# Optimization experiments

Measured on AMD Instinct MI355X. Metric: run time of the kernel, lower is better.

The kernel has to match this reference:

```python
import jax, jax.numpy as jnp
import numpy as np

NH = 8      # num_head
WIN = 7     # window
EPS = 1e-6


def _ln(x, w, b):
    m = x.mean(-1, keepdims=True)
    v = ((x - m) ** 2).mean(-1, keepdims=True)
    return (x - m) / jnp.sqrt(v + EPS) * w + b


def _dwconv(x, w, b):
    # x: [B,H,W,Cc], w: [7,7,1,Cc] (HWIO), depthwise (groups=Cc)
    y = jax.lax.conv_general_dilated(
        x, w, window_strides=(1, 1), padding='SAME',
        dimension_numbers=('NHWC', 'HWIO', 'NHWC'),
        feature_group_count=x.shape[-1])
    return y + b


def setup_inputs() -> dict:
    B, H, W, C = 16, 56, 56, 256
    RATIO = 8
    key = jax.random.key(0)
    ki = iter(jax.random.split(key, 48))
    def lin(i, o):
        return jax.random.normal(next(ki), (i, o), jnp.float32) * (1.0 / i) ** 0.5
    def bias(o):
        return jnp.zeros((o,), jnp.float32)
    def dw(c):
        return jax.random.normal(next(ki), (7, 7, 1, c), jnp.float32) * 0.05
    inp = {
        'x':   jax.random.normal(next(ki), (B, H, W, C), jnp.float32),
        'x_e': jax.random.normal(next(ki), (B, H, W, C // 2), jnp.float32),
        # LayerNorms
        'norm_w': jnp.ones((C,), jnp.float32),  'norm_b': bias(C),
        'norme_w': jnp.ones((C // 2,), jnp.float32), 'norme_b': bias(C // 2),
        # local_rr path
        'rr1_w': lin(C, C), 'rr1_b': bias(C),
        'rr2_w': lin(C, C), 'rr2_b': bias(C),
        'rr3_w': lin(C, C), 'rr3_b': bias(C),
        'conv_w': dw(C), 'conv_b': bias(C),
        # LocalAttentionRGBT
        'lx_l1_w': lin(C, C // 2), 'lx_l1_b': bias(C // 2),
        'lx_l2_w': lin(C // 2, C // 2), 'lx_l2_b': bias(C // 2),
        'lx_c1_w': dw(C // 2), 'lx_c1_b': bias(C // 2),
        'lx_c2_w': dw(C // 2), 'lx_c2_b': bias(C // 2),
        'lx_fc1_w': lin(C, C // RATIO),  # no bias
        'lx_fc2_w': lin(C // RATIO, C),  # no bias
        'lx_l3_w': lin(C, C // 2), 'lx_l3_b': bias(C // 2),
        # global pooled attention
        'kv_w': lin(C, C), 'kv_b': bias(C),
        'q_w': lin(C // 2 * 3, C // 2), 'q_b': bias(C // 2),
        # output projections (window != 0 => in = 2C)
        'proj_w': lin(2 * C, C), 'proj_b': bias(C),
        'proje_w': lin(2 * C, C // 2), 'proje_b': bias(C // 2),
    }
    return inp


def reference(x, x_e, norm_w, norm_b, norme_w, norme_b,
              rr1_w, rr1_b, rr2_w, rr2_b, rr3_w, rr3_b, conv_w, conv_b,
              lx_l1_w, lx_l1_b, lx_l2_w, lx_l2_b, lx_c1_w, lx_c1_b,
              lx_c2_w, lx_c2_b, lx_fc1_w, lx_fc2_w, lx_l3_w, lx_l3_b,
              kv_w, kv_b, q_w, q_b, proj_w, proj_b, proje_w, proje_b):
    B, H, W, C = x.shape
    hd = C // NH // 2  # head dim
    x = _ln(x, norm_w, norm_b)
    x_e = _ln(x_e, norme_w, norme_b)

    # --- local_rr: gated depthwise-conv branch ---
    rr1 = x @ rr1_w + rr1_b
    rr2 = _dwconv(x @ rr2_w + rr2_b, conv_w, conv_b)
    rr2 = rr2 @ rr3_w + rr3_b
    local_rr = rr1 * rr2  # [B,H,W,C]

    # --- LocalAttentionRGBT: cross-modal cosine-sim channel gate ---
    rgb = x @ lx_l1_w + lx_l1_b      # [B,H,W,C/2]
    t = x_e @ lx_l2_w + lx_l2_b      # [B,H,W,C/2]
    co = _dwconv(rgb * t, lx_c1_w, lx_c1_b)
    di = _dwconv(jnp.abs(rgb - t), lx_c2_w, lx_c2_b)
    co_di = jnp.concatenate([co, di], axis=-1)           # [B,H,W,C]
    amap = co_di.mean(-1, keepdims=True)                 # [B,H,W,1]
    dot = (amap * co_di).sum((1, 2), keepdims=True)      # [B,1,1,C]
    n1 = jnp.sqrt((amap ** 2).sum((1, 2), keepdims=True))
    n2 = jnp.sqrt((co_di ** 2).sum((1, 2), keepdims=True))
    cos_sim = dot / (n1 * n2 + 1e-6)                     # [B,1,1,C]
    attn_c = jax.nn.sigmoid(
        jax.nn.gelu(cos_sim @ lx_fc1_w, approximate=False) @ lx_fc2_w)
    local_rx = (co_di * attn_c) @ lx_l3_w + lx_l3_b      # [B,H,W,C/2]

    # --- global: pooled-q full-kv attention ---
    kv = (x @ kv_w + kv_b).reshape(B, H * W, 2, NH, hd).transpose(2, 0, 3, 1, 4)
    k, v = kv[0], kv[1]                                  # [B,NH,HW,hd]
    rx = jnp.concatenate([x, x_e], axis=-1)              # [B,H,W,3C/2]
    rx_pool = rx.reshape(B, WIN, H // WIN, WIN, W // WIN, -1).mean((2, 4))  # [B,7,7,3C/2]
    q = (rx_pool @ q_w + q_b).reshape(B, WIN * WIN, NH, hd).transpose(0, 2, 1, 3)
    scores = jnp.einsum('bnqd,bnkd->bnqk', q * hd ** -0.5, k)  # [B,NH,49,HW]
    attn = jax.nn.softmax(scores, axis=-1)
    g = jnp.einsum('bnqk,bnkd->bnqd', attn, v)           # [B,NH,49,hd]
    g = g.reshape(B, NH, WIN, WIN, hd).transpose(0, 1, 4, 2, 3).reshape(B, C // 2, WIN, WIN)
    g = jax.image.resize(g, (B, C // 2, H, W), method='bilinear')  # align_corners=False
    g = g.transpose(0, 2, 3, 1)                          # [B,H,W,C/2]

    cat = jnp.concatenate([local_rr, local_rx, g], axis=-1)  # [B,H,W,2C]
    x_e_out = cat @ proje_w + proje_b
    x_out = cat @ proj_w + proj_b
    return (x_out, x_e_out)
```

## Files before the change

### kernel.cpp

```cpp
#include <hip/hip_runtime.h>
#include <hip/hip_bf16.h>
#include <cstdint>
#include <cstddef>

#define N_TOK 50176
#define HWSZ  3136
#define BATCH 16

#define GF_MUL     1
#define GF_ASCALE  2
#define GF_KVSPLIT 4
#define GF_DUAL    8
#define GF_TRI     16
#define GF_RGBT    32

typedef __hip_bfloat16 bf16;
typedef __attribute__((ext_vector_type(8))) short bf16x8;
typedef __attribute__((ext_vector_type(4))) float f32x4;
typedef __attribute__((ext_vector_type(4))) unsigned short u16x4;

__device__ __forceinline__ void  stf(float* p, size_t i, float v) { p[i] = v; }
__device__ __forceinline__ void  stf(bf16* p, size_t i, float v) { p[i] = __float2bfloat16(v); }
__device__ __forceinline__ float bu2f(unsigned short u) {
    unsigned int x = ((unsigned int)u) << 16; float f; __builtin_memcpy(&f, &x, 4); return f;
}
__device__ __forceinline__ unsigned short f2bu(float f) {
    bf16 t = __float2bfloat16(f); unsigned short u; __builtin_memcpy(&u, &t, 2); return u;
}

struct WtrDesc { const float* src; bf16* dst; int K; int N; int off; };
struct WtrPack { WtrDesc d[9]; int total; };
__global__ __launch_bounds__(256) void wtr_all(WtrPack p)
{
    int idx = blockIdx.x * 256 + threadIdx.x;
    if (idx >= p.total) return;
    #pragma unroll
    for (int s = 0; s < 9; s++) {
        int lo = p.d[s].off, hi = lo + p.d[s].K * p.d[s].N;
        if (idx >= lo && idx < hi) {
            int j = idx - lo;
            int k = j / p.d[s].N, n = j % p.d[s].N;
            p.d[s].dst[(size_t)n * p.d[s].K + k] = __float2bfloat16(p.d[s].src[j]);
        }
    }
}

__global__ __launch_bounds__(256) void ln_kernel(const float* __restrict__ in,
    const float* __restrict__ w, const float* __restrict__ b,
    bf16* __restrict__ out, int rows, int Cdim)
{
    int wave = threadIdx.x >> 6, lane = threadIdx.x & 63;
    int row = blockIdx.x * 4 + wave;
    if (row >= rows) return;
    const float* p = in + (size_t)row * Cdim;
    int nj = Cdim >> 6;
    float v[4];
    float s = 0.f;
    for (int j = 0; j < nj; j++) { v[j] = p[lane + 64 * j]; s += v[j]; }
    for (int off = 32; off; off >>= 1) s += __shfl_xor(s, off, 64);
    float mean = s / (float)Cdim;
    float vs = 0.f;
    for (int j = 0; j < nj; j++) { float d = v[j] - mean; vs += d * d; }
    for (int off = 32; off; off >>= 1) vs += __shfl_xor(vs, off, 64);
    float rstd = 1.f / sqrtf(vs / (float)Cdim + 1e-6f);
    bf16* q = out + (size_t)row * Cdim;
    for (int j = 0; j < nj; j++) {
        int c = lane + 64 * j;
        q[c] = __float2bfloat16((v[j] - mean) * rstd * w[c] + b[c]);
    }
}

#define LDT 40
template<int FLAGS, typename OT>
__global__ __launch_bounds__(256) void gemm_mfma(
    const bf16* __restrict__ A, int lda,
    const bf16* __restrict__ WT,
    const float* __restrict__ bias,
    OT* __restrict__ C, int ldc,
    int M, int K, int N,
    const bf16* __restrict__ mul, int mulld,
    const float* __restrict__ ascale,
    bf16* __restrict__ kout, bf16* __restrict__ vout,
    OT* __restrict__ C2, int ldc2, const float* __restrict__ bias2, int N1)
{
    __shared__ bf16 As[2][64][LDT];
    __shared__ bf16 Bs[2][128][LDT];
    int ntile = N >> 7;
    int bid = blockIdx.x;
    bid = (bid & 7) * (gridDim.x >> 3) + (bid >> 3);
    int m0 = (bid / ntile) * 64;
    int n0 = (bid % ntile) * 128;
    int tid = threadIdx.x;
    int lane = tid & 63, wid = tid >> 6;
    int wc = wid * 32;
    int lrow = lane & 15, lko = (lane >> 4) * 8;
    int sr = tid >> 2, sko = (tid & 3) * 8;

    f32x4 acc[4][2];
    #pragma unroll
    for (int i = 0; i < 4; i++)
        #pragma unroll
        for (int j = 0; j < 2; j++)
            acc[i][j] = (f32x4){0.f, 0.f, 0.f, 0.f};

#define GLOAD(RA, RB0, RB1, KOFF) do {                                                        \
    bf16x8 v_ = *reinterpret_cast<const bf16x8*>(A + (size_t)(m0 + sr) * lda + (KOFF) + sko); \
    if (FLAGS & GF_ASCALE) {                                                                  \
        int bidx_ = (m0 + sr) / HWSZ;                                                         \
        const float* as_ = ascale + (size_t)bidx_ * K + (KOFF) + sko;                         \
        for (int e_ = 0; e_ < 8; e_++)                                                        \
            v_[e_] = (short)f2bu(bu2f((unsigned short)v_[e_]) * as_[e_]);                     \
    }                                                                                         \
    RA = v_;                                                                                  \
    RB0 = *reinterpret_cast<const bf16x8*>(WT + (size_t)(n0 + sr) * K + (KOFF) + sko);        \
    RB1 = *reinterpret_cast<const bf16x8*>(WT + (size_t)(n0 + sr + 64) * K + (KOFF) + sko);   \
} while (0)

#define GWRITE(P, RA, RB0, RB1) do {                                   \
    *reinterpret_cast<bf16x8*>(&As[P][sr][sko]) = RA;                  \
    *reinterpret_cast<bf16x8*>(&Bs[P][sr][sko]) = RB0;                 \
    *reinterpret_cast<bf16x8*>(&Bs[P][sr + 64][sko]) = RB1;            \
} while (0)

#define GCOMP(P) do {                                                                         \
    bf16x8 af_[4], br_[2];                                                                    \
    for (int i_ = 0; i_ < 4; i_++)                                                            \
        af_[i_] = *reinterpret_cast<const bf16x8*>(&As[P][i_ * 16 + lrow][lko]);              \
    for (int j_ = 0; j_ < 2; j_++)                                                            \
        br_[j_] = *reinterpret_cast<const bf16x8*>(&Bs[P][wc + j_ * 16 + lrow][lko]);         \
    for (int i_ = 0; i_ < 4; i_++)                                                            \
        for (int j_ = 0; j_ < 2; j_++)                                                        \
            acc[i_][j_] = __builtin_amdgcn_mfma_f32_16x16x32_bf16(af_[i_], br_[j_], acc[i_][j_], 0, 0, 0); \
} while (0)

    bf16x8 ra0, rb00, rb01, ra1, rb10, rb11;
    GLOAD(ra0, rb00, rb01, 0);
    GLOAD(ra1, rb10, rb11, 32);
    int nst = K >> 5;
    for (int s = 0; s < nst; s += 2) {
        GWRITE(0, ra0, rb00, rb01);
        if (s + 2 < nst) GLOAD(ra0, rb00, rb01, (s + 2) * 32);
        __syncthreads();
        GCOMP(0);
        GWRITE(1, ra1, rb10, rb11);
        if (s + 3 < nst) GLOAD(ra1, rb10, rb11, (s + 3) * 32);
        __syncthreads();
        GCOMP(1);
    }
#undef GLOAD
#undef GWRITE
#undef GCOMP

    int orow = (lane >> 4) * 4;
    int ocol = lane & 15;
    #pragma unroll
    for (int i = 0; i < 4; i++) {
        #pragma unroll
        for (int j = 0; j < 2; j++) {
            #pragma unroll
            for (int p = 0; p < 4; p++) {
                int gm = m0 + i * 16 + orow + p;
                int gn = n0 + wc + j * 16 + ocol;
                if (FLAGS & GF_TRI) {
                    if (gn < 256) {
                        stf(C, (size_t)gm * ldc + gn, acc[i][j][p] + bias[gn]);
                    } else if (gn < 512) {
                        stf(C2, (size_t)gm * ldc2 + (gn - 256), acc[i][j][p] + bias2[gn - 256]);
                    } else {
                        int g3 = gn - 512;
                        float v = acc[i][j][p] + ascale[g3];
                        int bb = gm / HWSZ, n = gm % HWSZ;
                        if (g3 < 128)
                            kout[(((size_t)bb * 8 + (g3 >> 4)) * HWSZ + n) * 16 + (g3 & 15)] = __float2bfloat16(v);
                        else {
                            int hh = (g3 - 128) >> 4, dd = (g3 - 128) & 15;
                            vout[(((size_t)bb * 8 + hh) * 16 + dd) * HWSZ + n] = __float2bfloat16(v);
                        }
                    }
                } else if (FLAGS & GF_RGBT) {
                    float t = acc[i][j][p] + bias[gn];
                    float rgb = __bfloat162float(mul[(size_t)gm * mulld + gn]);
                    stf(C, (size_t)gm * ldc + gn, rgb * t);
                    stf(C, (size_t)gm * ldc + 128 + gn, fabsf(rgb - t));
                } else if (FLAGS & GF_KVSPLIT) {
                    float v = acc[i][j][p] + bias[gn];
                    int bb = gm / HWSZ, n = gm % HWSZ;
                    if (gn < 128)
                        kout[(((size_t)bb * 8 + (gn >> 4)) * HWSZ + n) * 16 + (gn & 15)] = __float2bfloat16(v);
                    else {
                        int hh = (gn - 128) >> 4, dd = (gn - 128) & 15;
                        vout[(((size_t)bb * 8 + hh) * 16 + dd) * HWSZ + n] = __float2bfloat16(v);
                    }
                } else if (FLAGS & GF_DUAL) {
                    if (gn < N1) {
                        float v = acc[i][j][p] + bias[gn];
                        stf(C, (size_t)gm * ldc + gn, v);
                    } else {
                        float v = acc[i][j][p] + bias2[gn - N1];
                        stf(C2, (size_t)gm * ldc2 + (gn - N1), v);
                    }
                } else {
                    float v = acc[i][j][p] + bias[gn];
                    if (FLAGS & GF_MUL) v *= __bfloat162float(mul[(size_t)gm * mulld + gn]);
                    stf(C, (size_t)gm * ldc + gn, v);
                }
            }
        }
    }
}

__global__ __launch_bounds__(256) void gemm_k(
    const float* __restrict__ A, int lda,
    const float* __restrict__ Wt, const float* __restrict__ bias,
    float* __restrict__ Cc, int ldc, int M, int K, int Nc)
{
    __shared__ float As[16][68];
    __shared__ float Ws[16][64];
    int ntile = Nc >> 6;
    int tile_n = blockIdx.x % ntile;
    int tile_m = blockIdx.x / ntile;
    int m0 = tile_m * 64, n0 = tile_n * 64;
    int tid = threadIdx.x;
    int tx = tid & 15, ty = tid >> 4;
    float acc[4][4] = {};
    for (int k0 = 0; k0 < K; k0 += 16) {
        int ks = tid & 15, ms = tid >> 4;
        #pragma unroll
        for (int i = 0; i < 4; i++) {
            int gm = m0 + ms + i * 16;
            As[ks][ms + i * 16] = (gm < M) ? A[(size_t)gm * lda + k0 + ks] : 0.f;
        }
        #pragma unroll
        for (int j = 0; j < 4; j++) {
            int k = (tid >> 6) * 4 + j;
            Ws[k][tid & 63] = Wt[(size_t)(k0 + k) * Nc + n0 + (tid & 63)];
        }
        __syncthreads();
        #pragma unroll
        for (int k = 0; k < 16; k++) {
            float a[4], w[4];
            #pragma unroll
            for (int i = 0; i < 4; i++) a[i] = As[k][ty * 4 + i];
            #pragma unroll
            for (int j = 0; j < 4; j++) w[j] = Ws[k][tx * 4 + j];
            #pragma unroll
            for (int i = 0; i < 4; i++)
                #pragma unroll
                for (int j = 0; j < 4; j++)
                    acc[i][j] += a[i] * w[j];
        }
        __syncthreads();
    }
    #pragma unroll
    for (int i = 0; i < 4; i++) {
        int gm = m0 + ty * 4 + i;
        if (gm >= M) continue;
        #pragma unroll
        for (int j = 0; j < 4; j++) {
            int gn = n0 + tx * 4 + j;
            Cc[(size_t)gm * ldc + gn] = acc[i][j] + bias[gn];
        }
    }
}

__global__ __launch_bounds__(256) void dwconv_reg(const bf16* __restrict__ in,
    bf16* __restrict__ out,
    const float* __restrict__ w0, const float* __restrict__ b0,
    const float* __restrict__ w1, const float* __restrict__ b1, int split)
{
    int tid = threadIdx.x;
    int chg = tid & 31;
    int bsw = (blockIdx.x & 7) * 196 + (blockIdx.x >> 3);
    int pg  = bsw * 8 + (tid >> 5);
    int xg = pg % 14;
    int y  = (pg / 14) % 56;
    int b  = pg / (14 * 56);
    int c0 = chg * 8;
    int x0 = xg * 4;

    const float* wp; const float* bp; int ws, cw;
    if (c0 < split) { wp = w0; bp = b0; ws = split;       cw = c0; }
    else            { wp = w1; bp = b1; ws = 256 - split; cw = c0 - split; }

    float acc[4][8];
    #pragma unroll
    for (int o = 0; o < 4; o++)
        #pragma unroll
        for (int e = 0; e < 8; e++) acc[o][e] = 0.f;

    const bf16* base = in + (size_t)b * HWSZ * 256 + c0;
    const float* wbase = wp + cw;
    #pragma unroll
    for (int ky = 0; ky < 7; ky++) {
        int gy = y + ky - 3;
        if (gy < 0 || gy >= 56) continue;
        const bf16* rowp = base + (size_t)gy * 56 * 256;
        float cf[10][8];
        #pragma unroll
        for (int j = 0; j < 10; j++) {
            int gx = x0 + j - 3;
            bf16x8 v = {0, 0, 0, 0, 0, 0, 0, 0};
            if ((unsigned)gx < 56u)
                v = *reinterpret_cast<const bf16x8*>(rowp + (size_t)gx * 256);
            #pragma unroll
            for (int e = 0; e < 8; e++) cf[j][e] = bu2f((unsigned short)v[e]);
        }
        const float* wrow = wbase + ky * 7 * ws;
        #pragma unroll
        for (int kx = 0; kx < 7; kx++) {
            float4 wa = *reinterpret_cast<const float4*>(wrow + kx * ws);
            float4 wb = *reinterpret_cast<const float4*>(wrow + kx * ws + 4);
            #pragma unroll
            for (int o = 0; o < 4; o++) {
                acc[o][0] += cf[o + kx][0] * wa.x;
                acc[o][1] += cf[o + kx][1] * wa.y;
                acc[o][2] += cf[o + kx][2] * wa.z;
                acc[o][3] += cf[o + kx][3] * wa.w;
                acc[o][4] += cf[o + kx][4] * wb.x;
                acc[o][5] += cf[o + kx][5] * wb.y;
                acc[o][6] += cf[o + kx][6] * wb.z;
                acc[o][7] += cf[o + kx][7] * wb.w;
            }
        }
    }

    float4 ba = *reinterpret_cast<const float4*>(bp + cw);
    float4 bb = *reinterpret_cast<const float4*>(bp + cw + 4);
    bf16* obase = out + (((size_t)b * HWSZ + (size_t)y * 56 + x0) * 256) + c0;
    #pragma unroll
    for (int o = 0; o < 4; o++) {
        bf16x8 ov;
        ov[0] = (short)f2bu(acc[o][0] + ba.x);
        ov[1] = (short)f2bu(acc[o][1] + ba.y);
        ov[2] = (short)f2bu(acc[o][2] + ba.z);
        ov[3] = (short)f2bu(acc[o][3] + ba.w);
        ov[4] = (short)f2bu(acc[o][4] + bb.x);
        ov[5] = (short)f2bu(acc[o][5] + bb.y);
        ov[6] = (short)f2bu(acc[o][6] + bb.z);
        ov[7] = (short)f2bu(acc[o][7] + bb.w);
        *reinterpret_cast<bf16x8*>(obase + (size_t)o * 256) = ov;
    }
}

__global__ __launch_bounds__(256) void cosred_k(const bf16* __restrict__ codi,
    float* __restrict__ part)
{
    int b = blockIdx.x >> 4;
    int bi = blockIdx.x & 15;
    int wave = threadIdx.x >> 6, lane = threadIdx.x & 63;
    int slot = bi * 4 + wave;
    float dloc[4] = {0,0,0,0}, n2loc[4] = {0,0,0,0};
    float n1loc = 0.f;
    for (int i = 0; i < 49; i++) {
        int p = slot * 49 + i;
        const bf16* row = codi + ((size_t)b * HWSZ + p) * 256;
        float v[4]; float sum = 0.f;
        #pragma unroll
        for (int j = 0; j < 4; j++) { v[j] = __bfloat162float(row[lane + 64 * j]); sum += v[j]; }
        for (int off = 32; off; off >>= 1) sum += __shfl_xor(sum, off, 64);
        float amap = sum * (1.f / 256.f);
        #pragma unroll
        for (int j = 0; j < 4; j++) { dloc[j] += amap * v[j]; n2loc[j] += v[j] * v[j]; }
        n1loc += amap * amap;
    }
    float* dst = part + ((size_t)b * 64 + slot) * 513;
    #pragma unroll
    for (int j = 0; j < 4; j++) {
        dst[lane + 64 * j] = dloc[j];
        dst[256 + lane + 64 * j] = n2loc[j];
    }
    if (lane == 0) dst[512] = n1loc;
}

__global__ __launch_bounds__(256) void mlp_kernel(const float* __restrict__ part,
    const float* __restrict__ fc1w, const float* __restrict__ fc2w,
    float* __restrict__ attnc)
{
    int b = blockIdx.x;
    int tid = threadIdx.x;
    __shared__ float cosb[256];
    __shared__ float hbuf[32];
    const float* pb = part + (size_t)b * 64 * 513;
    float dot = 0.f, n2 = 0.f, n1 = 0.f;
    for (int s = 0; s < 64; s++) {
        dot += pb[s * 513 + tid];
        n2  += pb[s * 513 + 256 + tid];
        n1  += pb[s * 513 + 512];
    }
    float cs = dot / (sqrtf(n1) * sqrtf(n2) + 1e-6f);
    cosb[tid] = cs;
    __syncthreads();
    if (tid < 32) {
        float h = 0.f;
        for (int c = 0; c < 256; c++) h += cosb[c] * fc1w[c * 32 + tid];
        h = 0.5f * h * (1.f + erff(h * 0.70710678f));
        hbuf[tid] = h;
    }
    __syncthreads();
    float o = 0.f;
    for (int j = 0; j < 32; j++) o += hbuf[j] * fc2w[j * 256 + tid];
    attnc[b * 256 + tid] = 1.f / (1.f + expf(-o));
}

__global__ __launch_bounds__(384) void pool_kernel(const bf16* __restrict__ xn,
    const bf16* __restrict__ xen, float* __restrict__ rxpool)
{
    int bij = blockIdx.x;
    int b = bij / 49; int ij = bij % 49; int i = ij / 7, j = ij % 7;
    int c = threadIdx.x;
    float s = 0.f;
    for (int dy = 0; dy < 8; dy++)
        for (int dx = 0; dx < 8; dx++) {
            size_t n = ((size_t)b * 56 + (i * 8 + dy)) * 56 + (j * 8 + dx);
            s += (c < 256) ? __bfloat162float(xn[n * 256 + c])
                           : __bfloat162float(xen[n * 128 + (c - 256)]);
        }
    rxpool[(size_t)bij * 384 + c] = s * (1.f / 64.f);
}

#define NSPLIT 14
#define POSB   224
__global__ __launch_bounds__(256) void attn_mfma(const float* __restrict__ qbuf,
    const bf16* __restrict__ kbuf, const bf16* __restrict__ vtbuf,
    float* __restrict__ osplit, float* __restrict__ mlbuf)
{
    int bh = blockIdx.x & 127;
    int split = blockIdx.x >> 7;
    int b = bh >> 3, h = bh & 7;
    int tid = threadIdx.x;
    int qt = tid >> 6;
    int lane = tid & 63;
    int lo = lane & 15, hi = lane >> 4;

    bf16x8 qf = {0, 0, 0, 0, 0, 0, 0, 0};
    int q = qt * 16 + lo;
    if (hi < 2 && q < 49) {
        const float* qp = qbuf + ((size_t)b * 49 + q) * 128 + h * 16 + hi * 8;
        #pragma unroll
        for (int j = 0; j < 8; j++) qf[j] = (short)f2bu(qp[j] * 0.25f);
    }
    const bf16* kbase = kbuf + (size_t)bh * HWSZ * 16;
    const bf16* vbase = vtbuf + ((size_t)bh * 16 + lo) * HWSZ;

    float m_run = -1e30f, l_run = 0.f;
    f32x4 oacc = {0.f, 0.f, 0.f, 0.f};
    int pos1 = 8 * (lo >> 2) + (lo & 3);
    const f32x4 zz = {0.f, 0.f, 0.f, 0.f};

    for (int t = 0; t < POSB / 32; t++) {
        int base = split * POSB + t * 32;
        bf16x8 kf1 = {0, 0, 0, 0, 0, 0, 0, 0}, kf2 = kf1;
        if (hi < 2) {
            kf1 = *reinterpret_cast<const bf16x8*>(kbase + (size_t)(base + pos1) * 16 + hi * 8);
            kf2 = *reinterpret_cast<const bf16x8*>(kbase + (size_t)(base + pos1 + 4) * 16 + hi * 8);
        }
        bf16x8 vf = *reinterpret_cast<const bf16x8*>(vbase + base + hi * 8);
        f32x4 s1 = __builtin_amdgcn_mfma_f32_16x16x32_bf16(kf1, qf, zz, 0, 0, 0);
        f32x4 s2 = __builtin_amdgcn_mfma_f32_16x16x32_bf16(kf2, qf, zz, 0, 0, 0);
        float pmax = fmaxf(fmaxf(fmaxf(s1[0], s1[1]), fmaxf(s1[2], s1[3])),
                           fmaxf(fmaxf(s2[0], s2[1]), fmaxf(s2[2], s2[3])));
        pmax = fmaxf(pmax, __shfl_xor(pmax, 16, 64));
        pmax = fmaxf(pmax, __shfl_xor(pmax, 32, 64));
        float mnew = fmaxf(m_run, pmax);
        float esc = __expf(m_run - mnew);
        l_run *= esc;
        float e0 = __shfl(esc, 4 * hi + 0, 64);
        float e1 = __shfl(esc, 4 * hi + 1, 64);
        float e2 = __shfl(esc, 4 * hi + 2, 64);
        float e3 = __shfl(esc, 4 * hi + 3, 64);
        oacc[0] *= e0; oacc[1] *= e1; oacc[2] *= e2; oacc[3] *= e3;
        float p0 = __expf(s1[0] - mnew), p1 = __expf(s1[1] - mnew);
        float p2 = __expf(s1[2] - mnew), p3 = __expf(s1[3] - mnew);
        float p4 = __expf(s2[0] - mnew), p5 = __expf(s2[1] - mnew);
        float p6 = __expf(s2[2] - mnew), p7 = __expf(s2[3] - mnew);
        float rs = ((p0 + p1) + (p2 + p3)) + ((p4 + p5) + (p6 + p7));
        rs += __shfl_xor(rs, 16, 64);
        rs += __shfl_xor(rs, 32, 64);
        l_run += rs;
        m_run = mnew;
        bf16x8 pf;
        pf[0] = (short)f2bu(p0); pf[1] = (short)f2bu(p1);
        pf[2] = (short)f2bu(p2); pf[3] = (short)f2bu(p3);
        pf[4] = (short)f2bu(p4); pf[5] = (short)f2bu(p5);
        pf[6] = (short)f2bu(p6); pf[7] = (short)f2bu(p7);
        oacc = __builtin_amdgcn_mfma_f32_16x16x32_bf16(pf, vf, oacc, 0, 0, 0);
    }

    float* ob = osplit + ((size_t)bh * NSPLIT + split) * 64 * 16;
    #pragma unroll
    for (int r = 0; r < 4; r++) {
        int qq = qt * 16 + 4 * hi + r;
        ob[(size_t)qq * 16 + lo] = oacc[r];
    }
    if (hi == 0) {
        float* mlb = mlbuf + (((size_t)bh * NSPLIT + split) * 64 + qt * 16 + lo) * 2;
        mlb[0] = m_run; mlb[1] = l_run;
    }
}

__global__ __launch_bounds__(256) void attn_combine(const float* __restrict__ osplit,
    const float* __restrict__ mlbuf, float* __restrict__ gs)
{
    int idx = blockIdx.x * 256 + threadIdx.x;
    if (idx >= 128 * 49 * 16) return;
    int d = idx & 15;
    int pq = idx >> 4;
    int bh = pq / 49, q = pq % 49;
    float m[NSPLIT], l[NSPLIT];
    float M = -1e30f;
    #pragma unroll
    for (int s = 0; s < NSPLIT; s++) {
        const float* mlb = mlbuf + (((size_t)bh * NSPLIT + s) * 64 + q) * 2;
        m[s] = mlb[0]; l[s] = mlb[1];
        M = fmaxf(M, m[s]);
    }
    float L = 0.f, O = 0.f;
    #pragma unroll
    for (int s = 0; s < NSPLIT; s++) {
        float e = __expf(m[s] - M);
        L += l[s] * e;
        O += osplit[(((size_t)bh * NSPLIT + s) * 64 + q) * 16 + d] * e;
    }
    gs[(size_t)pq * 16 + d] = O / L;
}

__global__ void upsample_kernel(const float* __restrict__ gs, bf16* __restrict__ cat)
{
    int idx = blockIdx.x * blockDim.x + threadIdx.x;
    if (idx >= N_TOK * 128) return;
    int c = idx & 127;
    int pos = idx >> 7;
    int h = c >> 4, d = c & 15;
    int x = pos % 56;
    int y = (pos / 56) % 56;
    int b = pos / HWSZ;
    float sy = (y + 0.5f) * 0.125f - 0.5f;
    float sx = (x + 0.5f) * 0.125f - 0.5f;
    int y0f = (int)floorf(sy); float wy = sy - (float)y0f;
    int x0f = (int)floorf(sx); float wx = sx - (float)x0f;
    int y0 = max(0, min(6, y0f)), y1 = max(0, min(6, y0f + 1));
    int x0 = max(0, min(6, x0f)), x1 = max(0, min(6, x0f + 1));
    const float* g0 = gs + ((size_t)(b * 8 + h) * 49) * 16 + d;
    float v00 = g0[(y0 * 7 + x0) * 16], v01 = g0[(y0 * 7 + x1) * 16];
    float v10 = g0[(y1 * 7 + x0) * 16], v11 = g0[(y1 * 7 + x1) * 16];
    float v0 = v00 + (v01 - v00) * wx;
    float v1 = v10 + (v11 - v10) * wx;
    float v = v0 + (v1 - v0) * wy;
    cat[(size_t)pos * 512 + 384 + c] = __float2bfloat16(v);
}

extern "C" void kernel_launch(void* const* d_in, const int* in_sizes, int n_in,
                              void* d_out, int out_size, void* d_ws, size_t ws_size,
                              hipStream_t stream)
{
    const float* x      = (const float*)d_in[0];
    const float* x_e    = (const float*)d_in[1];
    const float* norm_w = (const float*)d_in[2];
    const float* norm_b = (const float*)d_in[3];
    const float* norme_w= (const float*)d_in[4];
    const float* norme_b= (const float*)d_in[5];
    const float* rr1_w  = (const float*)d_in[6];
    const float* rr1_b  = (const float*)d_in[7];
    const float* rr2_w  = (const float*)d_in[8];
    const float* rr2_b  = (const float*)d_in[9];
    const float* rr3_w  = (const float*)d_in[10];
    const float* rr3_b  = (const float*)d_in[11];
    const float* conv_w = (const float*)d_in[12];
    const float* conv_b = (const float*)d_in[13];
    const float* l1_w   = (const float*)d_in[14];
    const float* l1_b   = (const float*)d_in[15];
    const float* l2_w   = (const float*)d_in[16];
    const float* l2_b   = (const float*)d_in[17];
    const float* c1_w   = (const float*)d_in[18];
    const float* c1_b   = (const float*)d_in[19];
    const float* c2_w   = (const float*)d_in[20];
    const float* c2_b   = (const float*)d_in[21];
    const float* fc1_w  = (const float*)d_in[22];
    const float* fc2_w  = (const float*)d_in[23];
    const float* l3_w   = (const float*)d_in[24];
    const float* l3_b   = (const float*)d_in[25];
    const float* kv_w   = (const float*)d_in[26];
    const float* kv_b   = (const float*)d_in[27];
    const float* q_w    = (const float*)d_in[28];
    const float* q_b    = (const float*)d_in[29];
    const float* proj_w = (const float*)d_in[30];
    const float* proj_b = (const float*)d_in[31];
    const float* proje_w= (const float*)d_in[32];
    const float* proje_b= (const float*)d_in[33];

    float* part   = (float*)d_ws;
    float* attnc  = part   + (size_t)525312;
    float* gs     = attnc  + 4096;
    float* rxpool = gs     + 100352;
    float* qbuf   = rxpool + 301056;
    bf16* wt      = (bf16*)(qbuf + 100352);
    bf16* rr1_t  = wt;
    bf16* rr2_t  = rr1_t + 65536;
    bf16* kv_t   = rr2_t + 65536;
    bf16* rr3_t  = kv_t  + 65536;
    bf16* l1_t   = rr3_t + 65536;
    bf16* l2_t   = l1_t  + 32768;
    bf16* l3_t   = l2_t  + 16384;
    bf16* proj_t = l3_t  + 32768;
    bf16* proje_t= proj_t + 131072;
    bf16* xn     = proje_t + 65536;
    bf16* xen    = xn   + (size_t)N_TOK * 256;
    bf16* bufC   = xen  + (size_t)N_TOK * 128;
    bf16* bufD   = bufC + (size_t)N_TOK * 256;
    bf16* bufE   = bufD + (size_t)N_TOK * 256;
    bf16* cat    = bufE + (size_t)N_TOK * 256;
    bf16* kvbuf  = cat  + (size_t)N_TOK * 512;
    size_t need = (size_t)((char*)(kvbuf + (size_t)N_TOK * 256) - (char*)d_ws);
    if (ws_size < need) return;

    bf16* kbuf = kvbuf;
    bf16* vbuf = kvbuf + (size_t)N_TOK * 128;

    float* osplit = (float*)bufD;
    float* mlbuf  = osplit + (size_t)128 * NSPLIT * 64 * 16;

    float* xout  = (float*)d_out;
    float* xeout = xout + (size_t)N_TOK * 256;

    const int nthr = 256;
    auto mgrid = [](int M, int N) { return dim3((M / 64) * (N / 128)); };

    {
        WtrPack p;
        const float* srcs[9] = {rr1_w, rr2_w, kv_w, rr3_w, l1_w, l2_w, l3_w, proj_w, proje_w};
        bf16* dsts[9] = {rr1_t, rr2_t, kv_t, rr3_t, l1_t, l2_t, l3_t, proj_t, proje_t};
        int Ks[9] = {256, 256, 256, 256, 256, 128, 256, 512, 512};
        int Ns[9] = {256, 256, 256, 256, 128, 128, 128, 256, 128};
        int off = 0;
        for (int s = 0; s < 9; s++) {
            p.d[s] = {srcs[s], dsts[s], Ks[s], Ns[s], off};
            off += Ks[s] * Ns[s];
        }
        p.total = off;
        wtr_all<<<dim3((off + 255) / 256), dim3(256), 0, stream>>>(p);
    }

    ln_kernel<<<dim3(N_TOK / 4), dim3(nthr), 0, stream>>>(x, norm_w, norm_b, xn, N_TOK, 256);
    ln_kernel<<<dim3(N_TOK / 4), dim3(nthr), 0, stream>>>(x_e, norme_w, norme_b, xen, N_TOK, 128);

    gemm_mfma<GF_TRI, bf16><<<mgrid(N_TOK, 768), dim3(nthr), 0, stream>>>(
        xn, 256, rr1_t, rr1_b, bufC, 256, N_TOK, 256, 768, nullptr, 0, kv_b, kbuf, vbuf,
        bufD, 256, rr2_b, 0);
    dwconv_reg<<<dim3(N_TOK / 32), dim3(nthr), 0, stream>>>(
        bufD, bufE, conv_w, conv_b, conv_w, conv_b, 256);
    gemm_mfma<GF_MUL, bf16><<<mgrid(N_TOK, 256), dim3(nthr), 0, stream>>>(
        bufE, 256, rr3_t, rr3_b, cat, 512, N_TOK, 256, 256, bufC, 256, nullptr, nullptr, nullptr,
        nullptr, 0, nullptr, 0);

    gemm_mfma<0, bf16><<<mgrid(N_TOK, 128), dim3(nthr), 0, stream>>>(
        xn, 256, l1_t, l1_b, bufD, 128, N_TOK, 256, 128, nullptr, 0, nullptr, nullptr, nullptr,
        nullptr, 0, nullptr, 0);
    gemm_mfma<GF_RGBT, bf16><<<mgrid(N_TOK, 128), dim3(nthr), 0, stream>>>(
        xen, 128, l2_t, l2_b, bufC, 256, N_TOK, 128, 128, bufD, 128, nullptr, nullptr, nullptr,
        nullptr, 0, nullptr, 0);
    dwconv_reg<<<dim3(N_TOK / 32), dim3(nthr), 0, stream>>>(
        bufC, bufE, c1_w, c1_b, c2_w, c2_b, 128);
    cosred_k<<<dim3(BATCH * 16), dim3(nthr), 0, stream>>>(bufE, part);
    mlp_kernel<<<dim3(BATCH), dim3(nthr), 0, stream>>>(part, fc1_w, fc2_w, attnc);
    gemm_mfma<GF_ASCALE, bf16><<<mgrid(N_TOK, 128), dim3(nthr), 0, stream>>>(
        bufE, 256, l3_t, l3_b, cat + 256, 512, N_TOK, 256, 128, nullptr, 0, attnc, nullptr, nullptr,
        nullptr, 0, nullptr, 0);

    pool_kernel<<<dim3(BATCH * 49), dim3(384), 0, stream>>>(xn, xen, rxpool);
    gemm_k<<<dim3(((784 + 63) / 64) * 2), dim3(nthr), 0, stream>>>(
        rxpool, 384, q_w, q_b, qbuf, 128, 784, 384, 128);
    attn_mfma<<<dim3(128 * NSPLIT), dim3(nthr), 0, stream>>>(qbuf, kbuf, vbuf, osplit, mlbuf);
    attn_combine<<<dim3(392), dim3(nthr), 0, stream>>>(osplit, mlbuf, gs);
    upsample_kernel<<<dim3((N_TOK * 128) / nthr), dim3(nthr), 0, stream>>>(gs, cat);

    gemm_mfma<GF_DUAL, float><<<mgrid(N_TOK, 384), dim3(nthr), 0, stream>>>(
        cat, 512, proj_t, proj_b, xout, 256, N_TOK, 512, 384, nullptr, 0, nullptr, nullptr, nullptr,
        xeout, 128, proje_b, 256);
}
```

Before: 423.4 us.

## Load GEMM weight fragments directly into registers instead of via LDS

The MFMA GEMM no longer stages the weight (B) tile in shared memory. Each wave now reads its own 32-column B fragments straight from global memory into registers, prefetching one k-step ahead, and only the A tile still goes through LDS. This removes the B-tile LDS writes and reads and halves LDS use, and the A-tile padding shrinks from 40 to 36. In exchange, B global reads become strided 16-byte loads per lane that rely on cache hits, and the 72-byte LDS row stride may break 16-byte alignment of the vector LDS accesses.

```diff
diff --git a/kernel.cpp b/kernel.cpp
--- a/kernel.cpp
+++ b/kernel.cpp
@@ -70,7 +70,7 @@
     }
 }
 
-#define LDT 40
+#define LDT 36
 template<int FLAGS, typename OT>
 __global__ __launch_bounds__(256) void gemm_mfma(
     const bf16* __restrict__ A, int lda,
@@ -84,7 +84,6 @@
     OT* __restrict__ C2, int ldc2, const float* __restrict__ bias2, int N1)
 {
     __shared__ bf16 As[2][64][LDT];
-    __shared__ bf16 Bs[2][128][LDT];
     int ntile = N >> 7;
     int bid = blockIdx.x;
     bid = (bid & 7) * (gridDim.x >> 3) + (bid >> 3);
@@ -103,7 +102,7 @@
         for (int j = 0; j < 2; j++)
             acc[i][j] = (f32x4){0.f, 0.f, 0.f, 0.f};
 
-#define GLOAD(RA, RB0, RB1, KOFF) do {                                                        \
+#define ALOAD(RA, KOFF) do {                                                                  \
     bf16x8 v_ = *reinterpret_cast<const bf16x8*>(A + (size_t)(m0 + sr) * lda + (KOFF) + sko); \
     if (FLAGS & GF_ASCALE) {                                                                  \
         int bidx_ = (m0 + sr) / HWSZ;                                                         \
@@ -112,43 +111,56 @@
             v_[e_] = (short)f2bu(bu2f((unsigned short)v_[e_]) * as_[e_]);                     \
     }                                                                                         \
     RA = v_;                                                                                  \
-    RB0 = *reinterpret_cast<const bf16x8*>(WT + (size_t)(n0 + sr) * K + (KOFF) + sko);        \
-    RB1 = *reinterpret_cast<const bf16x8*>(WT + (size_t)(n0 + sr + 64) * K + (KOFF) + sko);   \
 } while (0)
 
-#define GWRITE(P, RA, RB0, RB1) do {                                   \
-    *reinterpret_cast<bf16x8*>(&As[P][sr][sko]) = RA;                  \
-    *reinterpret_cast<bf16x8*>(&Bs[P][sr][sko]) = RB0;                 \
-    *reinterpret_cast<bf16x8*>(&Bs[P][sr + 64][sko]) = RB1;            \
-} while (0)
-
-#define GCOMP(P) do {                                                                         \
-    bf16x8 af_[4], br_[2];                                                                    \
+#define GCOMP(P, B0, B1) do {                                                                 \
+    bf16x8 af_[4];                                                                            \
     for (int i_ = 0; i_ < 4; i_++)                                                            \
         af_[i_] = *reinterpret_cast<const bf16x8*>(&As[P][i_ * 16 + lrow][lko]);              \
-    for (int j_ = 0; j_ < 2; j_++)                                                            \
-        br_[j_] = *reinterpret_cast<const bf16x8*>(&Bs[P][wc + j_ * 16 + lrow][lko]);         \
-    for (int i_ = 0; i_ < 4; i_++)                                                            \
-        for (int j_ = 0; j_ < 2; j_++)                                                        \
-            acc[i_][j_] = __builtin_amdgcn_mfma_f32_16x16x32_bf16(af_[i_], br_[j_], acc[i_][j_], 0, 0, 0); \
+    for (int i_ = 0; i_ < 4; i_++) {                                                          \
+        acc[i_][0] = __builtin_amdgcn_mfma_f32_16x16x32_bf16(af_[i_], B0, acc[i_][0], 0, 0, 0); \
+        acc[i_][1] = __builtin_amdgcn_mfma_f32_16x16x32_bf16(af_[i_], B1, acc[i_][1], 0, 0, 0); \
+    }                                                                                         \
 } while (0)
 
-    bf16x8 ra0, rb00, rb01, ra1, rb10, rb11;
-    GLOAD(ra0, rb00, rb01, 0);
-    GLOAD(ra1, rb10, rb11, 32);
+    const bf16* bp0 = WT + (size_t)(n0 + wc + lrow) * K + lko;
+    const bf16* bp1 = WT + (size_t)(n0 + wc + 16 + lrow) * K + lko;
+
+    bf16x8 ra0, ra1;
+    ALOAD(ra0, 0);
+    ALOAD(ra1, 32);
+    bf16x8 bc0 = *reinterpret_cast<const bf16x8*>(bp0);
+    bf16x8 bc1 = *reinterpret_cast<const bf16x8*>(bp1);
     int nst = K >> 5;
     for (int s = 0; s < nst; s += 2) {
-        GWRITE(0, ra0, rb00, rb01);
-        if (s + 2 < nst) GLOAD(ra0, rb00, rb01, (s + 2) * 32);
+        *reinterpret_cast<bf16x8*>(&As[0][sr][sko]) = ra0;
+        if (s + 2 < nst) ALOAD(ra0, (s + 2) * 32);
+        bf16x8 bn0 = bc0, bn1 = bc1;
+        {
+            int kn = (s + 1) * 32;
+            if (kn < K) {
+                bn0 = *reinterpret_cast<const bf16x8*>(bp0 + kn);
+                bn1 = *reinterpret_cast<const bf16x8*>(bp1 + kn);
+            }
+        }
         __syncthreads();
-        GCOMP(0);
-        GWRITE(1, ra1, rb10, rb11);
-        if (s + 3 < nst) GLOAD(ra1, rb10, rb11, (s + 3) * 32);
+        GCOMP(0, bc0, bc1);
+        *reinterpret_cast<bf16x8*>(&As[1][sr][sko]) = ra1;
+        if (s + 3 < nst) ALOAD(ra1, (s + 3) * 32);
+        bc0 = bn0; bc1 = bn1;
+        bn0 = bc0; bn1 = bc1;
+        {
+            int kn = (s + 2) * 32;
+            if (kn < K) {
+                bn0 = *reinterpret_cast<const bf16x8*>(bp0 + kn);
+                bn1 = *reinterpret_cast<const bf16x8*>(bp1 + kn);
+            }
+        }
         __syncthreads();
-        GCOMP(1);
-    }
-#undef GLOAD
-#undef GWRITE
+        GCOMP(1, bc0, bc1);
+        bc0 = bn0; bc1 = bn1;
+    }
+#undef ALOAD
 #undef GCOMP
 
     int orow = (lane >> 4) * 4;
```

New measurement: 455.8 us. +7.6%, slower.
